# Kernel optimization log

Hardware: AMD Instinct MI355X
Metric: run time of the kernel (lower is better)

## Reference

```python
import jax, jax.numpy as jnp
import numpy as np

B, S, E, NW = 16, 4096, 512, 8  # batch, seq, embed_dim, n_wires (=d_k)
H = E // NW  # num_heads = 64


def setup_inputs() -> dict:
    key = jax.random.key(0)
    ks = jax.random.split(key, 10)
    s = 1.0 / np.sqrt(E)
    return {
        "x": jax.random.normal(ks[0], (B, S, E), dtype=jnp.float32),
        "Wq": jax.random.normal(ks[1], (E, E), dtype=jnp.float32) * s,
        "bq": jnp.zeros((E,), dtype=jnp.float32),
        "Wk": jax.random.normal(ks[2], (E, E), dtype=jnp.float32) * s,
        "bk": jnp.zeros((E,), dtype=jnp.float32),
        "Wv": jax.random.normal(ks[3], (E, E), dtype=jnp.float32) * s,
        "bv": jnp.zeros((E,), dtype=jnp.float32),
        "Wo": jax.random.normal(ks[4], (E, E), dtype=jnp.float32) * s,
        "bo": jnp.zeros((E,), dtype=jnp.float32),
        "theta": jax.random.normal(ks[5], (NW,), dtype=jnp.float32) * 0.1,
    }


def reference(x, Wq, bq, Wk, bk, Wv, bv, Wo, bo, theta):
    b, s, e = x.shape
    h, dk = H, NW

    def qproj(t):
        # Quantum circuit on product state: RX(t_i) then RX(theta_i) on wire i,
        # measure PauliZ -> <Z_i> = cos(t_i + theta_i). Shape [B,S,H,NW].
        return jnp.cos(t.reshape(b, s, h, dk) + theta)

    q = qproj(x @ Wq.T + bq)
    k = qproj(x @ Wk.T + bk)
    v = qproj(x @ Wv.T + bv)

    # Faithful to original: tensors enter attention as [B, S, H, dk], so the
    # softmax attention is computed ACROSS HEADS for each token position.
    scale = 1.0 / np.sqrt(dk)
    scores = jnp.einsum("bsid,bsjd->bsij", q, k) * scale  # [B,S,H,H]
    p = jax.nn.softmax(scores, axis=-1)
    out = jnp.einsum("bsij,bsjd->bsid", p, v)  # [B,S,H,dk]

    # out.transpose(1,2).contiguous().view(B,-1,E) from the torch code
    out = jnp.transpose(out, (0, 2, 1, 3)).reshape(b, -1, e)
    return out @ Wo.T + bo
```

## Files before the change

### kernel.cpp

```cpp
#include <hip/hip_runtime.h>
#include <hip/hip_bf16.h>
#include <math.h>


typedef __attribute__((ext_vector_type(8))) short short8;
typedef __attribute__((ext_vector_type(4))) float floatx4;

static __device__ __forceinline__ unsigned short f2bf(float f) {
  unsigned u = __float_as_uint(f);
  u += 0x7fffu + ((u >> 16) & 1u);
  return (unsigned short)(u >> 16);
}
static __device__ __forceinline__ float bf2f(unsigned short h) {
  return __uint_as_float(((unsigned)h) << 16);
}

static __device__ __forceinline__ void gload16(const void* g, void* l) {
  __builtin_amdgcn_global_load_lds(
      (const __attribute__((address_space(1))) void*)g,
      (__attribute__((address_space(3))) void*)l, 16, 0, 0);
}

__global__ void cvt_kernel(const float* __restrict__ in, unsigned short* __restrict__ out, int n) {
  int i0 = (blockIdx.x * blockDim.x + threadIdx.x) * 4;
  int stride = gridDim.x * blockDim.x * 4;
  for (int i = i0; i < n; i += stride) {
    const float4 v = *reinterpret_cast<const float4*>(in + i);
    ushort4 o;
    o.x = f2bf(v.x); o.y = f2bf(v.y); o.z = f2bf(v.z); o.w = f2bf(v.w);
    *reinterpret_cast<ushort4*>(out + i) = o;
  }
}

template<int MODE, int NBLK>
__global__ __launch_bounds__(256, 1) void gemm_kernel(
    const unsigned short* __restrict__ A,
    const unsigned short* __restrict__ W0,
    const float* __restrict__ b0,
    const float* __restrict__ b1,
    const float* __restrict__ b2,
    const float* __restrict__ theta,
    unsigned short* __restrict__ o0,
    float* __restrict__ outF)
{
  __shared__ unsigned short As[128 * 64];
  __shared__ unsigned short Bs[128 * 64];

  const int tid = threadIdx.x;
  const int bid = blockIdx.x;
  const int m_blk = bid / NBLK;
  const int n_blk = bid - m_blk * NBLK;
  const int m0 = m_blk << 7;

  const unsigned short* W;
  const float* bias;
  int n0, wsel = 0;
  if constexpr (MODE == 0) {
    wsel = n_blk >> 2;
    n0 = (n_blk & 3) << 7;
    W = W0 + (size_t)wsel * 262144;
    bias = (wsel == 0) ? b0 : ((wsel == 1) ? b1 : b2);
  } else {
    W = W0; bias = b0; n0 = n_blk << 7;
  }

  const int lane = tid & 63;
  const int w = tid >> 6;
  const int wm = (w >> 1) << 6;
  const int wn = (w & 1) << 6;
  const int lr = lane & 15;
  const int kg = lane >> 4;

  const int srow = lane >> 3;
  const int scol = (lane & 7) << 3;

  floatx4 acc[4][4] = {};

  for (int k0 = 0; k0 < 512; k0 += 64) {
    #pragma unroll
    for (int i = 0; i < 4; ++i) {
      const int chunk = (i << 2) | w;
      const int row = (chunk << 3) + srow;
      gload16(&A[(size_t)(m0 + row) * 512 + k0 + scol], &As[chunk << 9]);
      gload16(&W[(size_t)(n0 + row) * 512 + k0 + scol], &Bs[chunk << 9]);
    }
    __syncthreads();

    #pragma unroll
    for (int kk = 0; kk < 64; kk += 32) {
      short8 af[4], bfr[4];
      #pragma unroll
      for (int mi = 0; mi < 4; ++mi)
        af[mi] = *reinterpret_cast<const short8*>(&As[(wm + mi * 16 + lr) * 64 + kk + kg * 8]);
      #pragma unroll
      for (int ni = 0; ni < 4; ++ni)
        bfr[ni] = *reinterpret_cast<const short8*>(&Bs[(wn + ni * 16 + lr) * 64 + kk + kg * 8]);
      #pragma unroll
      for (int mi = 0; mi < 4; ++mi)
        #pragma unroll
        for (int ni = 0; ni < 4; ++ni)
          acc[mi][ni] = __builtin_amdgcn_mfma_f32_16x16x32_bf16(af[mi], bfr[ni], acc[mi][ni], 0, 0, 0);
    }
    __syncthreads();
  }

  float bl[4];
  #pragma unroll
  for (int ni = 0; ni < 4; ++ni) bl[ni] = bias[n0 + wn + ni * 16 + lr];
  float thl = 0.0f;
  if constexpr (MODE == 0) thl = theta[lr & 7];

  #pragma unroll
  for (int mi = 0; mi < 4; ++mi) {
    #pragma unroll
    for (int ni = 0; ni < 4; ++ni) {
      #pragma unroll
      for (int i = 0; i < 4; ++i) {
        int gm = m0 + wm + mi * 16 + kg * 4 + i;
        int gn = n0 + wn + ni * 16 + lr;
        float val = acc[mi][ni][i] + bl[ni];
        if constexpr (MODE == 0) {
          o0[(size_t)wsel * 33554432 + (size_t)gm * 512 + gn] = f2bf(cosf(val + thl));
        } else {
          outF[(size_t)gm * 512 + gn] = val;
        }
      }
    }
  }
}

__global__ __launch_bounds__(256) void attn_kernel(
    const unsigned short* __restrict__ q,
    const unsigned short* __restrict__ k,
    const unsigned short* __restrict__ v,
    unsigned short* __restrict__ out)
{
  __shared__ float kf[4][64][9];
  __shared__ float vf[4][64][9];
  const int w = threadIdx.x >> 6;
  const int lane = threadIdx.x & 63;
  const int t = blockIdx.x * 4 + w;

  const size_t base = (size_t)t * 512 + lane * 8;
  short8 q8 = *reinterpret_cast<const short8*>(q + base);
  short8 k8 = *reinterpret_cast<const short8*>(k + base);
  short8 v8 = *reinterpret_cast<const short8*>(v + base);

  float qf[8];
  #pragma unroll
  for (int d = 0; d < 8; ++d) {
    qf[d] = bf2f((unsigned short)q8[d]);
    kf[w][lane][d] = bf2f((unsigned short)k8[d]);
    vf[w][lane][d] = bf2f((unsigned short)v8[d]);
  }
  __syncthreads();

  float s[64];
  #pragma unroll
  for (int j = 0; j < 64; ++j) {
    float a = 0.f;
    #pragma unroll
    for (int d = 0; d < 8; ++d) a += qf[d] * kf[w][j][d];
    s[j] = a;
  }
  float m = s[0];
  #pragma unroll
  for (int j = 1; j < 64; ++j) m = fmaxf(m, s[j]);

  const float c = 0.35355339059327f * 1.44269504089f;
  float o[8] = {0, 0, 0, 0, 0, 0, 0, 0};
  float sum = 0.f;
  #pragma unroll
  for (int j = 0; j < 64; ++j) {
    float p = exp2f((s[j] - m) * c);
    sum += p;
    #pragma unroll
    for (int d = 0; d < 8; ++d) o[d] += p * vf[w][j][d];
  }
  const float inv = 1.0f / sum;

  const int b = t >> 12;
  const int sidx = t & 4095;
  const int sb = sidx >> 6, si = sidx & 63;
  const size_t row = (size_t)(b << 12) + (lane << 6) + sb;
  short8 o8;
  #pragma unroll
  for (int d = 0; d < 8; ++d) o8[d] = (short)f2bf(o[d] * inv);
  *reinterpret_cast<short8*>(out + row * 512 + si * 8) = o8;
}

extern "C" void kernel_launch(void* const* d_in, const int* in_sizes, int n_in,
                              void* d_out, int out_size, void* d_ws, size_t ws_size,
                              hipStream_t stream) {
  const float* x     = (const float*)d_in[0];
  const float* Wq    = (const float*)d_in[1];
  const float* bq    = (const float*)d_in[2];
  const float* Wk    = (const float*)d_in[3];
  const float* bk    = (const float*)d_in[4];
  const float* Wv    = (const float*)d_in[5];
  const float* bv    = (const float*)d_in[6];
  const float* Wo    = (const float*)d_in[7];
  const float* bo    = (const float*)d_in[8];
  const float* theta = (const float*)d_in[9];
  float* out = (float*)d_out;

  char* ws = (char*)d_ws;
  const size_t MB = 1024ull * 1024ull;
  unsigned short* xb  = (unsigned short*)(ws);
  unsigned short* qb  = (unsigned short*)(ws + 64 * MB);
  unsigned short* wqb = (unsigned short*)(ws + 256 * MB);
  unsigned short* wkb = wqb + 262144;
  unsigned short* wvb = wqb + 524288;
  unsigned short* wob = wqb + 786432;

  const int NX = 65536 * 512;
  const int NW2 = 512 * 512;

  cvt_kernel<<<2048, 256, 0, stream>>>(x, xb, NX);
  cvt_kernel<<<256, 256, 0, stream>>>(Wq, wqb, NW2);
  cvt_kernel<<<256, 256, 0, stream>>>(Wk, wkb, NW2);
  cvt_kernel<<<256, 256, 0, stream>>>(Wv, wvb, NW2);
  cvt_kernel<<<256, 256, 0, stream>>>(Wo, wob, NW2);

  gemm_kernel<0, 12><<<6144, 256, 0, stream>>>(xb, wqb, bq, bk, bv, theta, qb, nullptr);

  attn_kernel<<<16384, 256, 0, stream>>>(qb, qb + 33554432, qb + 67108864, xb);

  gemm_kernel<1, 4><<<2048, 256, 0, stream>>>(xb, wob, bo, nullptr, nullptr, nullptr, nullptr, out);
}
```

Measured before the change: 2.019 ms.

## Swizzle LDS, stage coalesced epilogues, remap blocks, batch attention tokens, fuse weight casts

```diff
diff --git a/kernel.cpp b/kernel.cpp
--- a/kernel.cpp
+++ b/kernel.cpp
@@ -32,8 +32,25 @@
   }
 }
 
+__global__ void cvt4_kernel(const float* __restrict__ w0, const float* __restrict__ w1,
+                            const float* __restrict__ w2, const float* __restrict__ w3,
+                            unsigned short* __restrict__ out) {
+  const int wsel = blockIdx.x >> 6;
+  const float* src = (wsel == 0) ? w0 : (wsel == 1) ? w1 : (wsel == 2) ? w2 : w3;
+  const int base = (blockIdx.x & 63) * 4096 + threadIdx.x * 4;
+  unsigned short* dst = out + wsel * 262144;
+  #pragma unroll
+  for (int it = 0; it < 4; ++it) {
+    int i = base + it * 1024;
+    const float4 v = *reinterpret_cast<const float4*>(src + i);
+    ushort4 o;
+    o.x = f2bf(v.x); o.y = f2bf(v.y); o.z = f2bf(v.z); o.w = f2bf(v.w);
+    *reinterpret_cast<ushort4*>(dst + i) = o;
+  }
+}
+
 template<int MODE, int NBLK>
-__global__ __launch_bounds__(256, 1) void gemm_kernel(
+__global__ __launch_bounds__(256) void gemm_kernel(
     const unsigned short* __restrict__ A,
     const unsigned short* __restrict__ W0,
     const float* __restrict__ b0,
@@ -43,14 +60,21 @@
     unsigned short* __restrict__ o0,
     float* __restrict__ outF)
 {
-  __shared__ unsigned short As[128 * 64];
-  __shared__ unsigned short Bs[128 * 64];
+  constexpr int STAGE_BYTES = (MODE == 0) ? (4 * 64 * 72 * 2) : (4 * 64 * 72 * 4);
+  constexpr int SMEM_BYTES = (STAGE_BYTES > 32768) ? STAGE_BYTES : 32768;
+  __shared__ __align__(16) char smem[SMEM_BYTES];
+  unsigned short* As = (unsigned short*)smem;
+  unsigned short* Bs = As + 128 * 64;
 
   const int tid = threadIdx.x;
   const int bid = blockIdx.x;
-  const int m_blk = bid / NBLK;
-  const int n_blk = bid - m_blk * NBLK;
-  const int m0 = m_blk << 7;
+
+  const int x = bid & 7;
+  const int i_in = bid >> 3;
+  int m_local, n_blk;
+  if constexpr (MODE == 0) { m_local = i_in / 12; n_blk = i_in - m_local * 12; }
+  else                     { m_local = i_in >> 2; n_blk = i_in & 3; }
+  const int m0 = ((x << 6) + m_local) << 7;
 
   const unsigned short* W;
   const float* bias;
@@ -70,9 +94,10 @@
   const int wn = (w & 1) << 6;
   const int lr = lane & 15;
   const int kg = lane >> 4;
+  const int r7a = lr & 7;
 
   const int srow = lane >> 3;
-  const int scol = (lane & 7) << 3;
+  const int scol = ((lane & 7) ^ srow) << 3;
 
   floatx4 acc[4][4] = {};
 
@@ -91,10 +116,12 @@
       short8 af[4], bfr[4];
       #pragma unroll
       for (int mi = 0; mi < 4; ++mi)
-        af[mi] = *reinterpret_cast<const short8*>(&As[(wm + mi * 16 + lr) * 64 + kk + kg * 8]);
+        af[mi] = *reinterpret_cast<const short8*>(
+            &As[(wm + mi * 16 + lr) * 64 + (((kg + (kk >> 3)) ^ r7a) << 3)]);
       #pragma unroll
       for (int ni = 0; ni < 4; ++ni)
-        bfr[ni] = *reinterpret_cast<const short8*>(&Bs[(wn + ni * 16 + lr) * 64 + kk + kg * 8]);
+        bfr[ni] = *reinterpret_cast<const short8*>(
+            &Bs[(wn + ni * 16 + lr) * 64 + (((kg + (kk >> 3)) ^ r7a) << 3)]);
       #pragma unroll
       for (int mi = 0; mi < 4; ++mi)
         #pragma unroll
@@ -110,21 +137,41 @@
   float thl = 0.0f;
   if constexpr (MODE == 0) thl = theta[lr & 7];
 
-  #pragma unroll
-  for (int mi = 0; mi < 4; ++mi) {
-    #pragma unroll
-    for (int ni = 0; ni < 4; ++ni) {
-      #pragma unroll
-      for (int i = 0; i < 4; ++i) {
-        int gm = m0 + wm + mi * 16 + kg * 4 + i;
-        int gn = n0 + wn + ni * 16 + lr;
-        float val = acc[mi][ni][i] + bl[ni];
-        if constexpr (MODE == 0) {
-          o0[(size_t)wsel * 33554432 + (size_t)gm * 512 + gn] = f2bf(cosf(val + thl));
-        } else {
-          outF[(size_t)gm * 512 + gn] = val;
-        }
-      }
+  if constexpr (MODE == 0) {
+    unsigned short* st = (unsigned short*)smem + w * (64 * 72);
+    #pragma unroll
+    for (int mi = 0; mi < 4; ++mi)
+      #pragma unroll
+      for (int ni = 0; ni < 4; ++ni)
+        #pragma unroll
+        for (int i = 0; i < 4; ++i)
+          st[(mi * 16 + kg * 4 + i) * 72 + ni * 16 + lr] =
+              f2bf(cosf(acc[mi][ni][i] + bl[ni] + thl));
+    __syncthreads();
+    unsigned short* dst = o0 + (size_t)wsel * 33554432;
+    #pragma unroll
+    for (int p = 0; p < 8; ++p) {
+      const int rr = p * 8 + (lane >> 3);
+      const int cc = (lane & 7) << 3;
+      *reinterpret_cast<short8*>(&dst[(size_t)(m0 + wm + rr) * 512 + n0 + wn + cc]) =
+          *reinterpret_cast<const short8*>(&st[rr * 72 + cc]);
+    }
+  } else {
+    float* stf = (float*)smem + w * (64 * 72);
+    #pragma unroll
+    for (int mi = 0; mi < 4; ++mi)
+      #pragma unroll
+      for (int ni = 0; ni < 4; ++ni)
+        #pragma unroll
+        for (int i = 0; i < 4; ++i)
+          stf[(mi * 16 + kg * 4 + i) * 72 + ni * 16 + lr] = acc[mi][ni][i] + bl[ni];
+    __syncthreads();
+    #pragma unroll
+    for (int p = 0; p < 16; ++p) {
+      const int rr = p * 4 + (lane >> 4);
+      const int cc = (lane & 15) << 2;
+      *reinterpret_cast<float4*>(&outF[(size_t)(m0 + wm + rr) * 512 + n0 + wn + cc]) =
+          *reinterpret_cast<const float4*>(&stf[rr * 72 + cc]);
     }
   }
 }
@@ -137,56 +184,74 @@
 {
   __shared__ float kf[4][64][9];
   __shared__ float vf[4][64][9];
+  __shared__ unsigned short stg[64 * 128];
   const int w = threadIdx.x >> 6;
   const int lane = threadIdx.x & 63;
-  const int t = blockIdx.x * 4 + w;
-
-  const size_t base = (size_t)t * 512 + lane * 8;
-  short8 q8 = *reinterpret_cast<const short8*>(q + base);
-  short8 k8 = *reinterpret_cast<const short8*>(k + base);
-  short8 v8 = *reinterpret_cast<const short8*>(v + base);
-
-  float qf[8];
-  #pragma unroll
-  for (int d = 0; d < 8; ++d) {
-    qf[d] = bf2f((unsigned short)q8[d]);
-    kf[w][lane][d] = bf2f((unsigned short)k8[d]);
-    vf[w][lane][d] = bf2f((unsigned short)v8[d]);
-  }
-  __syncthreads();
-
-  float s[64];
-  #pragma unroll
-  for (int j = 0; j < 64; ++j) {
-    float a = 0.f;
-    #pragma unroll
-    for (int d = 0; d < 8; ++d) a += qf[d] * kf[w][j][d];
-    s[j] = a;
-  }
-  float m = s[0];
-  #pragma unroll
-  for (int j = 1; j < 64; ++j) m = fmaxf(m, s[j]);
-
-  const float c = 0.35355339059327f * 1.44269504089f;
-  float o[8] = {0, 0, 0, 0, 0, 0, 0, 0};
-  float sum = 0.f;
-  #pragma unroll
-  for (int j = 0; j < 64; ++j) {
-    float p = exp2f((s[j] - m) * c);
-    sum += p;
-    #pragma unroll
-    for (int d = 0; d < 8; ++d) o[d] += p * vf[w][j][d];
-  }
-  const float inv = 1.0f / sum;
-
-  const int b = t >> 12;
-  const int sidx = t & 4095;
-  const int sb = sidx >> 6, si = sidx & 63;
-  const size_t row = (size_t)(b << 12) + (lane << 6) + sb;
-  short8 o8;
-  #pragma unroll
-  for (int d = 0; d < 8; ++d) o8[d] = (short)f2bf(o[d] * inv);
-  *reinterpret_cast<short8*>(out + row * 512 + si * 8) = o8;
+  const int t0 = blockIdx.x * 16;
+
+  #pragma unroll
+  for (int it = 0; it < 4; ++it) {
+    const int si_l = w * 4 + it;
+    const int t = t0 + si_l;
+
+    const size_t base = (size_t)t * 512 + lane * 8;
+    short8 q8 = *reinterpret_cast<const short8*>(q + base);
+    short8 k8 = *reinterpret_cast<const short8*>(k + base);
+    short8 v8 = *reinterpret_cast<const short8*>(v + base);
+
+    float qf[8];
+    #pragma unroll
+    for (int d = 0; d < 8; ++d) {
+      qf[d] = bf2f((unsigned short)q8[d]);
+      kf[w][lane][d] = bf2f((unsigned short)k8[d]);
+      vf[w][lane][d] = bf2f((unsigned short)v8[d]);
+    }
+    __syncthreads();
+
+    float s[64];
+    #pragma unroll
+    for (int j = 0; j < 64; ++j) {
+      float a = 0.f;
+      #pragma unroll
+      for (int d = 0; d < 8; ++d) a += qf[d] * kf[w][j][d];
+      s[j] = a;
+    }
+    float m = s[0];
+    #pragma unroll
+    for (int j = 1; j < 64; ++j) m = fmaxf(m, s[j]);
+
+    const float c = 0.35355339059327f * 1.44269504089f;
+    float o[8] = {0, 0, 0, 0, 0, 0, 0, 0};
+    float sum = 0.f;
+    #pragma unroll
+    for (int j = 0; j < 64; ++j) {
+      float p = exp2f((s[j] - m) * c);
+      sum += p;
+      #pragma unroll
+      for (int d = 0; d < 8; ++d) o[d] += p * vf[w][j][d];
+    }
+    const float inv = 1.0f / sum;
+
+    short8 o8;
+    #pragma unroll
+    for (int d = 0; d < 8; ++d) o8[d] = (short)f2bf(o[d] * inv);
+    const int chunk = si_l ^ (lane & 7);
+    *reinterpret_cast<short8*>(&stg[lane * 128 + chunk * 8]) = o8;
+    __syncthreads();
+  }
+
+  const int b = t0 >> 12;
+  const int sidx = t0 & 4095;
+  const int sb = sidx >> 6;
+  const int g = (sidx >> 4) & 3;
+  #pragma unroll
+  for (int p = 0; p < 4; ++p) {
+    const int h = p * 16 + (threadIdx.x >> 4);
+    const int c = threadIdx.x & 15;
+    short8 val = *reinterpret_cast<const short8*>(&stg[h * 128 + (c ^ (h & 7)) * 8]);
+    const size_t row = (size_t)(b << 12) + (h << 6) + sb;
+    *reinterpret_cast<short8*>(&out[row * 512 + (g * 16 + c) * 8]) = val;
+  }
 }
 
 extern "C" void kernel_launch(void* const* d_in, const int* in_sizes, int n_in,
@@ -209,22 +274,15 @@
   unsigned short* xb  = (unsigned short*)(ws);
   unsigned short* qb  = (unsigned short*)(ws + 64 * MB);
   unsigned short* wqb = (unsigned short*)(ws + 256 * MB);
-  unsigned short* wkb = wqb + 262144;
-  unsigned short* wvb = wqb + 524288;
-  unsigned short* wob = wqb + 786432;
 
   const int NX = 65536 * 512;
-  const int NW2 = 512 * 512;
 
   cvt_kernel<<<2048, 256, 0, stream>>>(x, xb, NX);
-  cvt_kernel<<<256, 256, 0, stream>>>(Wq, wqb, NW2);
-  cvt_kernel<<<256, 256, 0, stream>>>(Wk, wkb, NW2);
-  cvt_kernel<<<256, 256, 0, stream>>>(Wv, wvb, NW2);
-  cvt_kernel<<<256, 256, 0, stream>>>(Wo, wob, NW2);
+  cvt4_kernel<<<256, 256, 0, stream>>>(Wq, Wk, Wv, Wo, wqb);
 
   gemm_kernel<0, 12><<<6144, 256, 0, stream>>>(xb, wqb, bq, bk, bv, theta, qb, nullptr);
 
-  attn_kernel<<<16384, 256, 0, stream>>>(qb, qb + 33554432, qb + 67108864, xb);
-
-  gemm_kernel<1, 4><<<2048, 256, 0, stream>>>(xb, wob, bo, nullptr, nullptr, nullptr, nullptr, out);
-}
+  attn_kernel<<<4096, 256, 0, stream>>>(qb, qb + 33554432, qb + 67108864, xb);
+
+  gemm_kernel<1, 4><<<2048, 256, 0, stream>>>(xb, wqb + 786432, bo, nullptr, nullptr, nullptr, nullptr, out);
+}
```

Measured after the change: 2.582 ms. 1.28x slower.
